# Kernel tuning notes

Hardware: AMD Instinct MI355X
Metric: run time of the kernel (lower is better)

The kernel has to match this reference:

```python
import jax, jax.numpy as jnp
import numpy as np

RESID = 1024
HEADS = 16
HEAD_DIM = 64


def setup_inputs() -> dict:
    key = jax.random.key(0)
    ks = jax.random.split(key, 6)
    B, S = 2, 2048
    residual_stream = jax.random.normal(ks[0], (B, S, RESID), dtype=jnp.float32)
    # per-head qkv linear params, stacked over heads: [H, resid, 3*head_dim]
    W_qkv = jax.random.normal(ks[1], (HEADS, RESID, 3 * HEAD_DIM), dtype=jnp.float32) * (1.0 / np.sqrt(RESID))
    b_qkv = jax.random.normal(ks[2], (HEADS, 3 * HEAD_DIM), dtype=jnp.float32) * 0.01
    # output projection resid -> resid
    W_o = jax.random.normal(ks[3], (RESID, RESID), dtype=jnp.float32) * (1.0 / np.sqrt(RESID))
    b_o = jax.random.normal(ks[4], (RESID,), dtype=jnp.float32) * 0.01
    return {"residual_stream": residual_stream, "W_qkv": W_qkv, "b_qkv": b_qkv, "W_o": W_o, "b_o": b_o}


def reference(residual_stream, W_qkv, b_qkv, W_o, b_o):
    # qkv per head: [B, H, S, 3*D]
    qkv = jnp.einsum('bsr,hrd->bhsd', residual_stream, W_qkv) + b_qkv[None, :, None, :]
    q = qkv[..., :HEAD_DIM]
    k = qkv[..., HEAD_DIM:2 * HEAD_DIM]
    v = qkv[..., 2 * HEAD_DIM:]
    # NOTE: original has no causal mask; softmax over full key axis
    scores = jnp.einsum('bhsd,bhtd->bhst', q, k) / jnp.sqrt(jnp.float32(HEAD_DIM))
    attn = jax.nn.softmax(scores, axis=-1)
    out = jnp.einsum('bhst,bhtd->bhsd', attn, v)  # [B, H, S, D]
    B, H, S, D = out.shape
    out = out.transpose(0, 2, 1, 3).reshape(B, S, H * D)  # concat heads -> [B, S, resid]
    return out @ W_o + b_o
```

## Files before the change

### kernel.cpp

```cpp
#include <hip/hip_runtime.h>
#include <hip/hip_bf16.h>

#define B_ 2
#define S_ 2048
#define H_ 16
#define HD 64
#define R_ 1024
#define N_ (B_*S_)

typedef unsigned short ushort_t;
typedef short bf16x8 __attribute__((ext_vector_type(8)));
typedef float f32x4 __attribute__((ext_vector_type(4)));
typedef float f32x16 __attribute__((ext_vector_type(16)));

#define MFMA(a,b,c) __builtin_amdgcn_mfma_f32_16x16x32_bf16(a,b,c,0,0,0)
#define MFMA32(a,b,c) __builtin_amdgcn_mfma_f32_32x32x16_bf16(a,b,c,0,0,0)
#define GLD16(g,l) __builtin_amdgcn_global_load_lds( \
    (const __attribute__((address_space(1))) void*)(g), \
    (__attribute__((address_space(3))) void*)(l), 16, 0, 0)

__device__ __forceinline__ unsigned short f2bf(float f) {
  unsigned int u = __builtin_bit_cast(unsigned int, f);
  u += 0x7fffu + ((u >> 16) & 1u);
  return (unsigned short)(u >> 16);
}

__device__ __forceinline__ unsigned int cvtpk(float lo, float hi) {
  unsigned int r;
  asm("v_cvt_pk_bf16_f32 %0, %1, %2" : "=v"(r) : "v"(lo), "v"(hi));
  return r;
}

__device__ __forceinline__ bf16x8 ld8(const ushort_t* p) {
  return *(const bf16x8*)p;
}

__global__ __launch_bounds__(256) void k_convert_x(const float* __restrict__ x,
                                                   ushort_t* __restrict__ xb) {
  int i = blockIdx.x * 256 + threadIdx.x;
  float4 v = ((const float4*)x)[i];
  ushort4 o;
  o.x = f2bf(v.x); o.y = f2bf(v.y); o.z = f2bf(v.z); o.w = f2bf(v.w);
  ((ushort4*)xb)[i] = o;
}

__global__ __launch_bounds__(256) void k_transpose(const float* __restrict__ in,
                                                   ushort_t* __restrict__ out,
                                                   int rows, int cols) {
  __shared__ float t[64][65];
  const size_t bo = (size_t)blockIdx.z * rows * cols;
  const int r0 = blockIdx.x * 64, c0 = blockIdx.y * 64;
  const int tx = threadIdx.x & 63, ty = threadIdx.x >> 6;
  #pragma unroll
  for (int i = 0; i < 16; i++) {
    int r = ty * 16 + i;
    t[r][tx] = in[bo + (size_t)(r0 + r) * cols + c0 + tx];
  }
  __syncthreads();
  #pragma unroll
  for (int i = 0; i < 16; i++) {
    int c = ty * 16 + i;
    out[bo + (size_t)(c0 + c) * rows + r0 + tx] = f2bf(t[tx][c]);
  }
}

__global__ __launch_bounds__(256, 2) void k_qkv(
    const ushort_t* __restrict__ Xb, const ushort_t* __restrict__ WT,
    const float* __restrict__ bqkv,
    ushort_t* __restrict__ Q, ushort_t* __restrict__ K, ushort_t* __restrict__ Vt) {
  __shared__ ushort_t lA[2][128 * 32];
  __shared__ ushort_t lB[2][192 * 32];
  const int m0 = blockIdx.x * 128;
  const int h  = blockIdx.y;
  const int tid = threadIdx.x;
  const int w = tid >> 6, l = tid & 63;
  const int lr = l & 15, lg = l >> 4;
  const int wr = w >> 1, wc = w & 1;

  const ushort_t* Asrc = Xb + (size_t)m0 * R_;
  const ushort_t* Bsrc = WT + (size_t)h * 192 * R_;
  const int arow = l >> 2;
  const int acol = (l & 3) * 8;

  f32x4 acc[4][6];
  const f32x4 fz = {0.f, 0.f, 0.f, 0.f};
  #pragma unroll
  for (int m = 0; m < 4; m++)
    #pragma unroll
    for (int n = 0; n < 6; n++) acc[m][n] = fz;

  auto stage = [&](int buf, int kt) {
    const int k0 = kt * 32;
    #pragma unroll
    for (int i = 0; i < 2; i++) {
      int chunk = w + 4 * i;
      GLD16(Asrc + (size_t)(chunk * 16 + arow) * R_ + k0 + acol, &lA[buf][chunk * 512]);
    }
    #pragma unroll
    for (int i = 0; i < 3; i++) {
      int chunk = w + 4 * i;
      GLD16(Bsrc + (size_t)(chunk * 16 + arow) * R_ + k0 + acol, &lB[buf][chunk * 512]);
    }
  };

  stage(0, 0);
  asm volatile("s_waitcnt vmcnt(0)" ::: "memory");
  __syncthreads();

  int cur = 0;
  for (int kt = 0; kt < 32; ++kt) {
    if (kt < 31) stage(cur ^ 1, kt + 1);
    bf16x8 af[4], bfr[6];
    #pragma unroll
    for (int m = 0; m < 4; m++)
      af[m] = ld8(&lA[cur][(wr * 64 + m * 16 + lr) * 32 + lg * 8]);
    #pragma unroll
    for (int n = 0; n < 6; n++)
      bfr[n] = ld8(&lB[cur][(wc * 96 + n * 16 + lr) * 32 + lg * 8]);
    __builtin_amdgcn_s_setprio(1);
    #pragma unroll
    for (int m = 0; m < 4; m++)
      #pragma unroll
      for (int n = 0; n < 6; n++)
        acc[m][n] = MFMA(af[m], bfr[n], acc[m][n]);
    __builtin_amdgcn_s_setprio(0);
    asm volatile("s_waitcnt vmcnt(0)" ::: "memory");
    __syncthreads();
    cur ^= 1;
  }

  #pragma unroll
  for (int n = 0; n < 6; n++) {
    const int col = wc * 96 + n * 16 + lr;
    const float bias = bqkv[h * 192 + col];
    #pragma unroll
    for (int m = 0; m < 4; m++) {
      const int rb = m0 + wr * 64 + m * 16 + lg * 4;
      #pragma unroll
      for (int r = 0; r < 4; r++) {
        float v = acc[m][n][r] + bias;
        int srow = rb + r;
        int b = srow >> 11, s = srow & 2047;
        size_t bh = (size_t)b * H_ + h;
        if (col < 64) {
          Q[(bh * S_ + s) * HD + col] = f2bf(v * 0.1803368801111137f);
        } else if (col < 128) {
          int d = col - 64;
          K[(bh * S_ + s) * HD + (d ^ ((s & 7) << 3))] = f2bf(v);
        } else {
          int d = col - 128;
          Vt[(bh * HD + d) * S_ + (s ^ ((d & 7) << 3))] = f2bf(v);
        }
      }
    }
  }
}

__global__ __launch_bounds__(256, 2) void k_attn(
    const ushort_t* __restrict__ Q, const ushort_t* __restrict__ K,
    const ushort_t* __restrict__ Vt, ushort_t* __restrict__ AO) {
  __shared__ ushort_t lK[2][64 * 64];
  __shared__ ushort_t lV[2][64 * 64];
  const int qt = blockIdx.x;
  const int bh = blockIdx.y;
  const int b = bh >> 4, h = bh & 15;
  const int tid = threadIdx.x, w = tid >> 6, l = tid & 63;
  const int lq = l & 31, hi = l >> 5;

  const ushort_t* Qb = Q + (size_t)bh * S_ * HD;
  const ushort_t* Kb = K + (size_t)bh * S_ * HD;
  const ushort_t* Vb = Vt + (size_t)bh * HD * S_;

  bf16x8 qf[4];
  {
    int qrow = qt * 128 + 32 * w + lq;
    #pragma unroll
    for (int kd = 0; kd < 4; kd++)
      qf[kd] = ld8(&Qb[(size_t)qrow * HD + kd * 16 + hi * 8]);
  }

  auto stage = [&](int buf, int t0) {
    #pragma unroll
    for (int i = 0; i < 2; i++) {
      int chunk = w + 4 * i;
      int r = chunk * 8 + (l >> 3);
      int c = (l & 7) * 8;
      GLD16(&Kb[(size_t)(t0 + r) * HD + c], &lK[buf][chunk * 512]);
      GLD16(&Vb[(size_t)r * S_ + t0 + c], &lV[buf][chunk * 512]);
    }
  };

  const f32x16 fz16 = {0};
  const bf16x8 onesv = {0x3F80, 0x3F80, 0x3F80, 0x3F80, 0x3F80, 0x3F80, 0x3F80, 0x3F80};
  f32x16 oacc[2];
  f32x16 ss;
  oacc[0] = fz16; oacc[1] = fz16; ss = fz16;

  const int swz = (lq & 7) * 8;

  stage(0, 0);
  asm volatile("s_waitcnt vmcnt(0)" ::: "memory");
  __syncthreads();

  int cur = 0;
  for (int kt = 0; kt < 32; ++kt) {
    if (kt < 31) stage(cur ^ 1, (kt + 1) * 64);

    f32x16 sc[2];
    sc[0] = fz16; sc[1] = fz16;
    __builtin_amdgcn_s_setprio(1);
    #pragma unroll
    for (int kd = 0; kd < 4; kd++) {
      bf16x8 ka0 = ld8(&lK[cur][(lq) * 64 + ((kd * 16 + hi * 8) ^ swz)]);
      bf16x8 ka1 = ld8(&lK[cur][(32 + lq) * 64 + ((kd * 16 + hi * 8) ^ swz)]);
      sc[0] = MFMA32(ka0, qf[kd], sc[0]);
      sc[1] = MFMA32(ka1, qf[kd], sc[1]);
    }
    __builtin_amdgcn_s_setprio(0);

    unsigned int pk[2][4], pq[2][4], px[2][4], pxq[2][4];
    #pragma unroll
    for (int n = 0; n < 2; n++)
      #pragma unroll
      for (int b2 = 0; b2 < 4; b2++) {
        float e0 = exp2f(sc[n][4 * b2 + 0]);
        float e1 = exp2f(sc[n][4 * b2 + 1]);
        float e2 = exp2f(sc[n][4 * b2 + 2]);
        float e3 = exp2f(sc[n][4 * b2 + 3]);
        pk[n][b2] = cvtpk(e0, e1);
        pq[n][b2] = cvtpk(e2, e3);
      }
    #pragma unroll
    for (int n = 0; n < 2; n++)
      #pragma unroll
      for (int b2 = 0; b2 < 4; b2++) {
        px[n][b2]  = __shfl_xor((int)pk[n][b2], 32, 64);
        pxq[n][b2] = __shfl_xor((int)pq[n][b2], 32, 64);
      }

    __builtin_amdgcn_s_setprio(1);
    #pragma unroll
    for (int ks = 0; ks < 4; ks++) {
      const int n = ks >> 1, k1 = (ks & 1) * 2;
      unsigned int w0 = hi ? px[n][k1 + 1]  : pk[n][k1];
      unsigned int w1 = hi ? pxq[n][k1 + 1] : pq[n][k1];
      unsigned int w2 = hi ? pk[n][k1 + 1]  : px[n][k1];
      unsigned int w3 = hi ? pq[n][k1 + 1]  : pxq[n][k1];
      int4 wv = {(int)w0, (int)w1, (int)w2, (int)w3};
      bf16x8 pa = __builtin_bit_cast(bf16x8, wv);
      ss = MFMA32(pa, onesv, ss);
      #pragma unroll
      for (int db = 0; db < 2; db++) {
        bf16x8 vb = ld8(&lV[cur][(db * 32 + lq) * 64 + ((ks * 16 + hi * 8) ^ swz)]);
        oacc[db] = MFMA32(pa, vb, oacc[db]);
      }
    }
    __builtin_amdgcn_s_setprio(0);

    asm volatile("s_waitcnt vmcnt(0)" ::: "memory");
    __syncthreads();
    cur ^= 1;
  }

  float inv[16];
  #pragma unroll
  for (int reg = 0; reg < 16; reg++) inv[reg] = 1.0f / ss[reg];
  #pragma unroll
  for (int db = 0; db < 2; db++)
    #pragma unroll
    for (int reg = 0; reg < 16; reg++) {
      int qloc = (reg & 3) + 8 * (reg >> 2) + 4 * hi;
      int s = qt * 128 + 32 * w + qloc;
      float o = oacc[db][reg] * inv[reg];
      AO[(size_t)(b * S_ + s) * R_ + h * HD + db * 32 + lq] = f2bf(o);
    }
}

__global__ __launch_bounds__(256, 2) void k_out(
    const ushort_t* __restrict__ AO, const ushort_t* __restrict__ WoT,
    const float* __restrict__ bo, float* __restrict__ out) {
  __shared__ ushort_t lA[2][128 * 32];
  __shared__ ushort_t lB[2][128 * 32];
  const int m0 = blockIdx.x * 128, n0 = blockIdx.y * 128;
  const int tid = threadIdx.x, w = tid >> 6, l = tid & 63;
  const int lr = l & 15, lg = l >> 4;
  const int wr = w >> 1, wc = w & 1;
  const ushort_t* Asrc = AO + (size_t)m0 * R_;
  const ushort_t* Bsrc = WoT + (size_t)n0 * R_;
  const int arow = l >> 2, acol = (l & 3) * 8;

  f32x4 acc[4][4];
  const f32x4 fz = {0.f, 0.f, 0.f, 0.f};
  #pragma unroll
  for (int m = 0; m < 4; m++)
    #pragma unroll
    for (int n = 0; n < 4; n++) acc[m][n] = fz;

  auto stage = [&](int buf, int kt) {
    const int k0 = kt * 32;
    #pragma unroll
    for (int i = 0; i < 2; i++) {
      int chunk = w + 4 * i;
      GLD16(Asrc + (size_t)(chunk * 16 + arow) * R_ + k0 + acol, &lA[buf][chunk * 512]);
      GLD16(Bsrc + (size_t)(chunk * 16 + arow) * R_ + k0 + acol, &lB[buf][chunk * 512]);
    }
  };

  stage(0, 0);
  asm volatile("s_waitcnt vmcnt(0)" ::: "memory");
  __syncthreads();

  int cur = 0;
  for (int kt = 0; kt < 32; ++kt) {
    if (kt < 31) stage(cur ^ 1, kt + 1);
    bf16x8 af[4], bfr[4];
    #pragma unroll
    for (int m = 0; m < 4; m++)
      af[m] = ld8(&lA[cur][(wr * 64 + m * 16 + lr) * 32 + lg * 8]);
    #pragma unroll
    for (int n = 0; n < 4; n++)
      bfr[n] = ld8(&lB[cur][(wc * 64 + n * 16 + lr) * 32 + lg * 8]);
    __builtin_amdgcn_s_setprio(1);
    #pragma unroll
    for (int m = 0; m < 4; m++)
      #pragma unroll
      for (int n = 0; n < 4; n++)
        acc[m][n] = MFMA(af[m], bfr[n], acc[m][n]);
    __builtin_amdgcn_s_setprio(0);
    asm volatile("s_waitcnt vmcnt(0)" ::: "memory");
    __syncthreads();
    cur ^= 1;
  }

  #pragma unroll
  for (int n = 0; n < 4; n++) {
    const int col = n0 + wc * 64 + n * 16 + lr;
    const float bias = bo[col];
    #pragma unroll
    for (int m = 0; m < 4; m++) {
      const int row = m0 + wr * 64 + m * 16 + lg * 4;
      #pragma unroll
      for (int r = 0; r < 4; r++)
        out[(size_t)(row + r) * R_ + col] = acc[m][n][r] + bias;
    }
  }
}

extern "C" void kernel_launch(void* const* d_in, const int* in_sizes, int n_in,
                              void* d_out, int out_size, void* d_ws, size_t ws_size,
                              hipStream_t stream) {
  const float* resid = (const float*)d_in[0];
  const float* Wqkv  = (const float*)d_in[1];
  const float* bqkv  = (const float*)d_in[2];
  const float* Wo    = (const float*)d_in[3];
  const float* bo    = (const float*)d_in[4];
  float* out = (float*)d_out;

  ushort_t* Xb  = (ushort_t*)d_ws;
  ushort_t* WT  = Xb  + (size_t)N_ * R_;
  ushort_t* WoT = WT  + (size_t)H_ * 192 * R_;
  ushort_t* Qd  = WoT + (size_t)R_ * R_;
  ushort_t* Kd  = Qd  + (size_t)B_ * H_ * S_ * HD;
  ushort_t* Vtd = Kd  + (size_t)B_ * H_ * S_ * HD;
  ushort_t* AOd = Vtd + (size_t)B_ * H_ * S_ * HD;

  k_convert_x<<<dim3(4096), dim3(256), 0, stream>>>(resid, Xb);
  k_transpose<<<dim3(16, 3, 16), dim3(256), 0, stream>>>(Wqkv, WT, 1024, 192);
  k_transpose<<<dim3(16, 16, 1), dim3(256), 0, stream>>>(Wo, WoT, 1024, 1024);
  k_qkv<<<dim3(32, 16), dim3(256), 0, stream>>>(Xb, WT, bqkv, Qd, Kd, Vtd);
  k_attn<<<dim3(16, 32), dim3(256), 0, stream>>>(Qd, Kd, Vtd, AOd);
  k_out<<<dim3(32, 8), dim3(256), 0, stream>>>(AOd, WoT, bo, out);
}
```

Measured before the change: 140.0 us.

## Stage K/V through registers with LDS swizzle and use permlane32 swap

The attention kernel now loads K and V tiles into registers and writes them to LDS with an XOR swizzle applied at store time, replacing direct global-to-LDS loads of pre-swizzled data. The QKV projection therefore writes K and Vt unswizzled. The P-matrix lane exchange uses v_permlane32_swap instead of shfl_xor plus selects, and the P·V MFMAs are interleaved with the exp/convert work per half. The aim is to cut bank conflicts and cross-lane shuffle overhead and to overlap softmax with matrix work, at the cost of extra VGPRs for the staging registers.

```diff
diff --git a/kernel.cpp b/kernel.cpp
--- a/kernel.cpp
+++ b/kernel.cpp
@@ -29,6 +29,10 @@
   unsigned int r;
   asm("v_cvt_pk_bf16_f32 %0, %1, %2" : "=v"(r) : "v"(lo), "v"(hi));
   return r;
+}
+
+__device__ __forceinline__ void plswap(unsigned int &a, unsigned int &b) {
+  asm volatile("v_permlane32_swap_b32 %0, %1" : "+v"(a), "+v"(b));
 }
 
 __device__ __forceinline__ bf16x8 ld8(const ushort_t* p) {
@@ -146,10 +150,10 @@
           Q[(bh * S_ + s) * HD + col] = f2bf(v * 0.1803368801111137f);
         } else if (col < 128) {
           int d = col - 64;
-          K[(bh * S_ + s) * HD + (d ^ ((s & 7) << 3))] = f2bf(v);
+          K[(bh * S_ + s) * HD + d] = f2bf(v);
         } else {
           int d = col - 128;
-          Vt[(bh * HD + d) * S_ + (s ^ ((d & 7) << 3))] = f2bf(v);
+          Vt[(bh * HD + d) * S_ + s] = f2bf(v);
         }
       }
     }
@@ -179,92 +183,90 @@
       qf[kd] = ld8(&Qb[(size_t)qrow * HD + kd * 16 + hi * 8]);
   }
 
-  auto stage = [&](int buf, int t0) {
+  const int sr = l >> 3;
+  const int scol = l & 7;
+  bf16x8 kreg[2], vreg[2];
+  auto issue = [&](int t0) {
     #pragma unroll
     for (int i = 0; i < 2; i++) {
-      int chunk = w + 4 * i;
-      int r = chunk * 8 + (l >> 3);
-      int c = (l & 7) * 8;
-      GLD16(&Kb[(size_t)(t0 + r) * HD + c], &lK[buf][chunk * 512]);
-      GLD16(&Vb[(size_t)r * S_ + t0 + c], &lV[buf][chunk * 512]);
+      int r = (w * 2 + i) * 8 + sr;
+      kreg[i] = ld8(&Kb[(size_t)(t0 + r) * HD + scol * 8]);
+      vreg[i] = ld8(&Vb[(size_t)r * S_ + t0 + scol * 8]);
+    }
+  };
+  auto commit = [&](int buf) {
+    #pragma unroll
+    for (int i = 0; i < 2; i++) {
+      int r = (w * 2 + i) * 8 + sr;
+      int off = r * 64 + ((scol ^ (r & 7)) * 8);
+      *(bf16x8*)&lK[buf][off] = kreg[i];
+      *(bf16x8*)&lV[buf][off] = vreg[i];
     }
   };
 
   const f32x16 fz16 = {0};
   const bf16x8 onesv = {0x3F80, 0x3F80, 0x3F80, 0x3F80, 0x3F80, 0x3F80, 0x3F80, 0x3F80};
   f32x16 oacc[2];
-  f32x16 ss;
-  oacc[0] = fz16; oacc[1] = fz16; ss = fz16;
-
-  const int swz = (lq & 7) * 8;
-
-  stage(0, 0);
-  asm volatile("s_waitcnt vmcnt(0)" ::: "memory");
+  f32x16 ssv;
+  oacc[0] = fz16; oacc[1] = fz16; ssv = fz16;
+
+  const int xr = lq & 7;
+
+  issue(0);
+  commit(0);
   __syncthreads();
 
   int cur = 0;
   for (int kt = 0; kt < 32; ++kt) {
-    if (kt < 31) stage(cur ^ 1, (kt + 1) * 64);
-
-    f32x16 sc[2];
-    sc[0] = fz16; sc[1] = fz16;
+    if (kt < 31) issue((kt + 1) * 64);
+
+    f32x16 sc0 = fz16, sc1 = fz16;
     __builtin_amdgcn_s_setprio(1);
     #pragma unroll
     for (int kd = 0; kd < 4; kd++) {
-      bf16x8 ka0 = ld8(&lK[cur][(lq) * 64 + ((kd * 16 + hi * 8) ^ swz)]);
-      bf16x8 ka1 = ld8(&lK[cur][(32 + lq) * 64 + ((kd * 16 + hi * 8) ^ swz)]);
-      sc[0] = MFMA32(ka0, qf[kd], sc[0]);
-      sc[1] = MFMA32(ka1, qf[kd], sc[1]);
+      bf16x8 ka0 = ld8(&lK[cur][lq * 64 + (((kd * 2 + hi) ^ xr) * 8)]);
+      bf16x8 ka1 = ld8(&lK[cur][(32 + lq) * 64 + (((kd * 2 + hi) ^ xr) * 8)]);
+      sc0 = MFMA32(ka0, qf[kd], sc0);
+      sc1 = MFMA32(ka1, qf[kd], sc1);
     }
     __builtin_amdgcn_s_setprio(0);
 
-    unsigned int pk[2][4], pq[2][4], px[2][4], pxq[2][4];
-    #pragma unroll
-    for (int n = 0; n < 2; n++)
-      #pragma unroll
-      for (int b2 = 0; b2 < 4; b2++) {
-        float e0 = exp2f(sc[n][4 * b2 + 0]);
-        float e1 = exp2f(sc[n][4 * b2 + 1]);
-        float e2 = exp2f(sc[n][4 * b2 + 2]);
-        float e3 = exp2f(sc[n][4 * b2 + 3]);
-        pk[n][b2] = cvtpk(e0, e1);
-        pq[n][b2] = cvtpk(e2, e3);
+    #pragma unroll
+    for (int n = 0; n < 2; n++) {
+      const f32x16 scv = n ? sc1 : sc0;
+      float e[16];
+      #pragma unroll
+      for (int r = 0; r < 16; r++) e[r] = exp2f(scv[r]);
+      #pragma unroll
+      for (int sl = 0; sl < 2; sl++) {
+        unsigned int X  = cvtpk(e[8 * sl + 0], e[8 * sl + 1]);
+        unsigned int Y  = cvtpk(e[8 * sl + 2], e[8 * sl + 3]);
+        unsigned int X2 = cvtpk(e[8 * sl + 4], e[8 * sl + 5]);
+        unsigned int Y2 = cvtpk(e[8 * sl + 6], e[8 * sl + 7]);
+        plswap(X, X2);
+        plswap(Y, Y2);
+        int4 wv = {(int)X, (int)Y, (int)X2, (int)Y2};
+        bf16x8 pa = __builtin_bit_cast(bf16x8, wv);
+        const int ks = n * 2 + sl;
+        __builtin_amdgcn_s_setprio(1);
+        ssv = MFMA32(pa, onesv, ssv);
+        #pragma unroll
+        for (int db = 0; db < 2; db++) {
+          bf16x8 vb = ld8(&lV[cur][(db * 32 + lq) * 64 + (((ks * 2 + hi) ^ xr) * 8)]);
+          oacc[db] = MFMA32(pa, vb, oacc[db]);
+        }
+        __builtin_amdgcn_s_setprio(0);
       }
-    #pragma unroll
-    for (int n = 0; n < 2; n++)
-      #pragma unroll
-      for (int b2 = 0; b2 < 4; b2++) {
-        px[n][b2]  = __shfl_xor((int)pk[n][b2], 32, 64);
-        pxq[n][b2] = __shfl_xor((int)pq[n][b2], 32, 64);
-      }
-
-    __builtin_amdgcn_s_setprio(1);
-    #pragma unroll
-    for (int ks = 0; ks < 4; ks++) {
-      const int n = ks >> 1, k1 = (ks & 1) * 2;
-      unsigned int w0 = hi ? px[n][k1 + 1]  : pk[n][k1];
-      unsigned int w1 = hi ? pxq[n][k1 + 1] : pq[n][k1];
-      unsigned int w2 = hi ? pk[n][k1 + 1]  : px[n][k1];
-      unsigned int w3 = hi ? pq[n][k1 + 1]  : pxq[n][k1];
-      int4 wv = {(int)w0, (int)w1, (int)w2, (int)w3};
-      bf16x8 pa = __builtin_bit_cast(bf16x8, wv);
-      ss = MFMA32(pa, onesv, ss);
-      #pragma unroll
-      for (int db = 0; db < 2; db++) {
-        bf16x8 vb = ld8(&lV[cur][(db * 32 + lq) * 64 + ((ks * 16 + hi * 8) ^ swz)]);
-        oacc[db] = MFMA32(pa, vb, oacc[db]);
-      }
-    }
-    __builtin_amdgcn_s_setprio(0);
-
-    asm volatile("s_waitcnt vmcnt(0)" ::: "memory");
+    }
+
+    if (kt < 31) commit(cur ^ 1);
     __syncthreads();
     cur ^= 1;
   }
 
   float inv[16];
   #pragma unroll
-  for (int reg = 0; reg < 16; reg++) inv[reg] = 1.0f / ss[reg];
+  for (int reg = 0; reg < 16; reg++) inv[reg] = 1.0f / ssv[reg];
   #pragma unroll
   for (int db = 0; db < 2; db++)
     #pragma unroll
```

Result: faster. 135.0 us (-3.6%).
